# Optimization experiments

Hardware: AMD Instinct MI355X
Metric: run time of the kernel (lower is better)

Reference implementation:

```python
import jax, jax.numpy as jnp
import numpy as np

N_NODES = 10000
N_EDGES = 320000
OBS_DIM = 30
ACT_DIM = 4
HID = 128


def setup_inputs() -> dict:
    key = jax.random.key(0)
    ks = jax.random.split(key, 16)

    def lin(k, fan_in, fan_out):
        s = 1.0 / np.sqrt(fan_in)
        kw, kb = jax.random.split(k)
        w = jax.random.uniform(kw, (fan_in, fan_out), jnp.float32, -s, s)
        b = jax.random.uniform(kb, (fan_out,), jnp.float32, -s, s)
        return w, b

    obs = jax.random.normal(ks[0], (N_NODES, OBS_DIM), jnp.float32)
    action = jax.random.normal(ks[1], (N_NODES, ACT_DIM), jnp.float32)
    edge_index = jax.random.randint(ks[2], (2, N_EDGES), 0, N_NODES, jnp.int64)

    w_g1, b_g1 = lin(ks[3], OBS_DIM + ACT_DIM, HID)
    w_g2, b_g2 = lin(ks[4], HID, HID)
    w_q1a, b_q1a = lin(ks[5], HID, HID)
    w_q1b, b_q1b = lin(ks[6], HID, 1)
    w_q2a, b_q2a = lin(ks[7], HID, HID)
    w_q2b, b_q2b = lin(ks[8], HID, 1)

    return dict(obs=obs, action=action, edge_index=edge_index,
                w_g1=w_g1, b_g1=b_g1, w_g2=w_g2, b_g2=b_g2,
                w_q1a=w_q1a, b_q1a=b_q1a, w_q1b=w_q1b, b_q1b=b_q1b,
                w_q2a=w_q2a, b_q2a=b_q2a, w_q2b=w_q2b, b_q2b=b_q2b)


def gcn_conv(x, w, b, src, dst, deg_inv_sqrt, n):
    xw = x @ w                                      # [N, Fout] small GEMM
    norm = deg_inv_sqrt[src] * deg_inv_sqrt[dst]    # [E'] edge norm
    msg = xw[src] * norm[:, None]                   # gather + scale, [E', Fout]
    out = jax.ops.segment_sum(msg, dst, num_segments=n)  # scatter-add
    return out + b


def reference(obs, action, edge_index,
              w_g1, b_g1, w_g2, b_g2,
              w_q1a, b_q1a, w_q1b, b_q1b,
              w_q2a, b_q2a, w_q2b, b_q2b):
    n = obs.shape[0]
    loops = jnp.arange(n, dtype=edge_index.dtype)
    src = jnp.concatenate([edge_index[0], loops])   # add self-loops
    dst = jnp.concatenate([edge_index[1], loops])

    deg = jnp.zeros((n,), jnp.float32).at[dst].add(1.0)
    deg_inv_sqrt = jnp.where(deg > 0, jax.lax.rsqrt(jnp.maximum(deg, 1.0)), 0.0)

    x = jnp.concatenate([obs, action], axis=1)
    x = jax.nn.relu(gcn_conv(x, w_g1, b_g1, src, dst, deg_inv_sqrt, n))
    x = jax.nn.relu(gcn_conv(x, w_g2, b_g2, src, dst, deg_inv_sqrt, n))

    q1 = jax.nn.relu(x @ w_q1a + b_q1a) @ w_q1b + b_q1b
    q2 = jax.nn.relu(x @ w_q2a + b_q2a) @ w_q2b + b_q2b
    return (q1, q2)
```

## Files before the change

kernel.cpp:

```cpp
#include <hip/hip_runtime.h>

#define N_NODES 10000
#define N_EDGES 320000
#define OBS_DIM 30
#define ACT_DIM 4
#define HID 128
#define ELL_W 96
#define SENT N_NODES


__global__ __launch_bounds__(256) void k_init(int* __restrict__ cnt,
                                              float* __restrict__ xpad,
                                              float* __restrict__ ph1,
                                              const float* __restrict__ obs,
                                              const float* __restrict__ act) {
    int i = blockIdx.x * 256 + threadIdx.x;
    if (i < (N_NODES + 1) * 16) {
        int row = i >> 4, sub = i & 15;
        float4 v = make_float4(0.f, 0.f, 0.f, 0.f);
        if (row < N_NODES) {
            float* vv = &v.x;
#pragma unroll
            for (int k = 0; k < 4; ++k) {
                int c = sub * 4 + k;
                if (c < OBS_DIM) vv[k] = obs[row * OBS_DIM + c];
                else if (c < OBS_DIM + ACT_DIM) vv[k] = act[row * ACT_DIM + (c - OBS_DIM)];
            }
        }
        ((float4*)xpad)[i] = v;
    }
    if (i <= N_NODES) cnt[i] = 0;
    if (i < HID / 4)
        ((float4*)(ph1 + (size_t)SENT * HID))[i] = make_float4(0.f, 0.f, 0.f, 0.f);
}


__global__ __launch_bounds__(256) void k_build(const int4* __restrict__ src4,
                                               const int4* __restrict__ dst4,
                                               int* __restrict__ cnt,
                                               int* __restrict__ col) {
    int i = blockIdx.x * 256 + threadIdx.x;
    if (i < N_EDGES / 4) {
        int4 s = src4[i];
        int4 d = dst4[i];
        int p;
        p = atomicAdd(&cnt[d.x], 1); col[d.x * ELL_W + p] = s.x;
        p = atomicAdd(&cnt[d.y], 1); col[d.y * ELL_W + p] = s.y;
        p = atomicAdd(&cnt[d.z], 1); col[d.z * ELL_W + p] = s.z;
        p = atomicAdd(&cnt[d.w], 1); col[d.w * ELL_W + p] = s.w;
    }
}


__global__ __launch_bounds__(512) void k_l1(const float4* __restrict__ x4,
                                            const int* __restrict__ cnt,
                                            const int* __restrict__ col,
                                            const float* __restrict__ W1,
                                            const float* __restrict__ b1,
                                            float* __restrict__ ph1) {
    __shared__ float w1s[34 * 128];
    __shared__ float zs[8][64];
    int t = threadIdx.x;
    {
        float4* wsp = (float4*)w1s;
        const float4* Wp = (const float4*)W1;
        for (int i = t; i < 1088; i += 512) wsp[i] = Wp[i];
    }
    __syncthreads();
    int wave = t >> 6, lane = t & 63, g = lane >> 4, sub = lane & 15;
    int node = blockIdx.x * 8 + wave;
    int deg = cnt[node];
    float di = rsqrtf((float)(deg + 1));
    const int* cp = col + node * ELL_W;
    float4 a = make_float4(0.f, 0.f, 0.f, 0.f);
    if (g == 0) {
        float4 xv = x4[node * 16 + sub];
        a.x = di * xv.x; a.y = di * xv.y; a.z = di * xv.z; a.w = di * xv.w;
    }
    for (int e = 0; e < deg; e += 8) {
        int s0 = e + g, s1 = e + 4 + g;
        int j0 = (s0 < deg) ? cp[s0] : SENT;
        int j1 = (s1 < deg) ? cp[s1] : SENT;
        float d0 = rsqrtf((float)(cnt[j0] + 1));
        float d1 = rsqrtf((float)(cnt[j1] + 1));
        float4 v0 = x4[j0 * 16 + sub];
        float4 v1 = x4[j1 * 16 + sub];
        a.x += d0 * v0.x + d1 * v1.x;
        a.y += d0 * v0.y + d1 * v1.y;
        a.z += d0 * v0.z + d1 * v1.z;
        a.w += d0 * v0.w + d1 * v1.w;
    }
    a.x += __shfl_xor(a.x, 16); a.x += __shfl_xor(a.x, 32);
    a.y += __shfl_xor(a.y, 16); a.y += __shfl_xor(a.y, 32);
    a.z += __shfl_xor(a.z, 16); a.z += __shfl_xor(a.z, 32);
    a.w += __shfl_xor(a.w, 16); a.w += __shfl_xor(a.w, 32);
    if (g == 0) {
        float4 z;
        z.x = di * a.x; z.y = di * a.y; z.z = di * a.z; z.w = di * a.w;
        *(float4*)&zs[wave][sub * 4] = z;
    }
    float h0 = b1[lane], h64 = b1[lane + 64];
#pragma unroll
    for (int k = 0; k < 34; ++k) {
        float zk = zs[wave][k];
        h0 += zk * w1s[k * 128 + lane];
        h64 += zk * w1s[k * 128 + 64 + lane];
    }
    ph1[node * HID + lane] = di * fmaxf(h0, 0.0f);
    ph1[node * HID + 64 + lane] = di * fmaxf(h64, 0.0f);
}


__global__ __launch_bounds__(256) void k_agg2(const float4* __restrict__ ph14,
                                              const int* __restrict__ cnt,
                                              const int* __restrict__ col,
                                              float4* __restrict__ sbuf) {
    int t = threadIdx.x;
    int wave = t >> 6, lane = t & 63, half = lane >> 5, sub = lane & 31;
    int node = blockIdx.x * 4 + wave;
    int deg = cnt[node];
    const int* cp = col + node * ELL_W;
    float4 a = make_float4(0.f, 0.f, 0.f, 0.f);
    float4 b = make_float4(0.f, 0.f, 0.f, 0.f);
    if (!half) a = ph14[node * 32 + sub];
    for (int e = 0; e < deg; e += 16) {
        int jj[8];
#pragma unroll
        for (int u = 0; u < 8; ++u) {
            int s = e + 2 * u + half;
            jj[u] = (s < deg) ? cp[s] : SENT;
        }
        float4 v0 = ph14[jj[0] * 32 + sub];
        float4 v1 = ph14[jj[1] * 32 + sub];
        float4 v2 = ph14[jj[2] * 32 + sub];
        float4 v3 = ph14[jj[3] * 32 + sub];
        float4 v4 = ph14[jj[4] * 32 + sub];
        float4 v5 = ph14[jj[5] * 32 + sub];
        float4 v6 = ph14[jj[6] * 32 + sub];
        float4 v7 = ph14[jj[7] * 32 + sub];
        a.x += (v0.x + v1.x) + (v2.x + v3.x);
        a.y += (v0.y + v1.y) + (v2.y + v3.y);
        a.z += (v0.z + v1.z) + (v2.z + v3.z);
        a.w += (v0.w + v1.w) + (v2.w + v3.w);
        b.x += (v4.x + v5.x) + (v6.x + v7.x);
        b.y += (v4.y + v5.y) + (v6.y + v7.y);
        b.z += (v4.z + v5.z) + (v6.z + v7.z);
        b.w += (v4.w + v5.w) + (v6.w + v7.w);
    }
    a.x += b.x; a.y += b.y; a.z += b.z; a.w += b.w;
    a.x += __shfl_xor(a.x, 32);
    a.y += __shfl_xor(a.y, 32);
    a.z += __shfl_xor(a.z, 32);
    a.w += __shfl_xor(a.w, 32);
    if (!half) sbuf[node * 32 + sub] = a;
}


__global__ __launch_bounds__(256) void k_h2heads(const float4* __restrict__ sbuf4,
                                                 const int* __restrict__ cnt,
                                                 const float* __restrict__ W2, const float* __restrict__ b2,
                                                 const float* __restrict__ Wq1, const float* __restrict__ Bq1,
                                                 const float* __restrict__ w1b, const float* __restrict__ b1b,
                                                 const float* __restrict__ Wq2, const float* __restrict__ Bq2,
                                                 const float* __restrict__ w2b, const float* __restrict__ b2b,
                                                 float* __restrict__ q1, float* __restrict__ q2) {
    __shared__ float xs[16 * 128];
    __shared__ float hs[16 * 128];
    __shared__ float wbA[32 * 128];
    __shared__ float wbB[32 * 128];
    __shared__ float part1[4][8], part2[4][8];
    int t = threadIdx.x;
    int row0 = blockIdx.x * 16;
    {
        float4* xsp = (float4*)xs;
        for (int i = t; i < 512; i += 256) xsp[i] = sbuf4[row0 * 32 + i];
    }
    int c = t & 127, q = t >> 7;
    float acc[8] = {0, 0, 0, 0, 0, 0, 0, 0};
    for (int ch = 0; ch < 4; ++ch) {
        __syncthreads();
        {
            float4* wp = (float4*)wbA;
            const float4* Wp = (const float4*)(W2 + ch * 4096);
            for (int i = t; i < 1024; i += 256) wp[i] = Wp[i];
        }
        __syncthreads();
        for (int k = 0; k < 32; ++k) {
            float wv = wbA[k * 128 + c];
#pragma unroll
            for (int r = 0; r < 8; ++r)
                acc[r] += xs[(q * 8 + r) * 128 + ch * 32 + k] * wv;
        }
    }
    {
        float bb = b2[c];
#pragma unroll
        for (int r = 0; r < 8; ++r) {
            int row = row0 + q * 8 + r;
            float dr = rsqrtf((float)(cnt[row] + 1));
            hs[(q * 8 + r) * 128 + c] = fmaxf(dr * acc[r] + bb, 0.0f);
        }
    }
    float a1[8] = {0, 0, 0, 0, 0, 0, 0, 0};
    float a2[8] = {0, 0, 0, 0, 0, 0, 0, 0};
    for (int ch = 0; ch < 4; ++ch) {
        __syncthreads();
        {
            float4* w1p = (float4*)wbA;
            float4* w2p = (float4*)wbB;
            const float4* W1p = (const float4*)(Wq1 + ch * 4096);
            const float4* W2p = (const float4*)(Wq2 + ch * 4096);
            for (int i = t; i < 1024; i += 256) {
                w1p[i] = W1p[i];
                w2p[i] = W2p[i];
            }
        }
        __syncthreads();
        for (int k = 0; k < 32; ++k) {
            float wv1 = wbA[k * 128 + c];
            float wv2 = wbB[k * 128 + c];
#pragma unroll
            for (int r = 0; r < 8; ++r) {
                float xv = hs[(q * 8 + r) * 128 + ch * 32 + k];
                a1[r] += xv * wv1;
                a2[r] += xv * wv2;
            }
        }
    }
    float bb1 = Bq1[c], bb2 = Bq2[c];
    float v1 = w1b[c], v2 = w2b[c];
    float s1[8], s2[8];
#pragma unroll
    for (int r = 0; r < 8; ++r) {
        s1[r] = fmaxf(a1[r] + bb1, 0.0f) * v1;
        s2[r] = fmaxf(a2[r] + bb2, 0.0f) * v2;
    }
#pragma unroll
    for (int off = 1; off < 64; off <<= 1) {
#pragma unroll
        for (int r = 0; r < 8; ++r) {
            s1[r] += __shfl_xor(s1[r], off);
            s2[r] += __shfl_xor(s2[r], off);
        }
    }
    int wave = t >> 6, lane = t & 63;
    if (lane == 0) {
#pragma unroll
        for (int r = 0; r < 8; ++r) {
            part1[wave][r] = s1[r];
            part2[wave][r] = s2[r];
        }
    }
    __syncthreads();
    if (t < 16) {
        int hf = t >> 3, r = t & 7;
        int row = row0 + hf * 8 + r;
        q1[row] = part1[hf * 2][r] + part1[hf * 2 + 1][r] + b1b[0];
        q2[row] = part2[hf * 2][r] + part2[hf * 2 + 1][r] + b2b[0];
    }
}

extern "C" void kernel_launch(void* const* d_in, const int* in_sizes, int n_in,
                              void* d_out, int out_size, void* d_ws, size_t ws_size,
                              hipStream_t stream) {
    (void)in_sizes; (void)n_in; (void)out_size; (void)ws_size;
    const float* obs  = (const float*)d_in[0];
    const float* act  = (const float*)d_in[1];
    const int*   ei   = (const int*)d_in[2];
    const int*   src  = ei;
    const int*   dst  = ei + N_EDGES;
    const float* w_g1 = (const float*)d_in[3];
    const float* b_g1 = (const float*)d_in[4];
    const float* w_g2 = (const float*)d_in[5];
    const float* b_g2 = (const float*)d_in[6];
    const float* w_q1a = (const float*)d_in[7];
    const float* b_q1a = (const float*)d_in[8];
    const float* w_q1b = (const float*)d_in[9];
    const float* b_q1b = (const float*)d_in[10];
    const float* w_q2a = (const float*)d_in[11];
    const float* b_q2a = (const float*)d_in[12];
    const float* w_q2b = (const float*)d_in[13];
    const float* b_q2b = (const float*)d_in[14];
    float* out = (float*)d_out;

    char* ws = (char*)d_ws;
    size_t off = 0;
    auto alloc = [&](size_t bytes) {
        void* p = ws + off;
        off = (off + bytes + 255) & ~(size_t)255;
        return p;
    };
    int*   cnt  = (int*)alloc((N_NODES + 1) * 4);
    int*   col  = (int*)alloc((size_t)N_NODES * ELL_W * 4);
    float* xpad = (float*)alloc((size_t)(N_NODES + 1) * 64 * 4);
    float* ph1  = (float*)alloc((size_t)(N_NODES + 1) * HID * 4);
    float* sbuf = (float*)alloc((size_t)N_NODES * HID * 4);

    k_init<<<((N_NODES + 1) * 16 + 255) / 256, 256, 0, stream>>>(cnt, xpad, ph1, obs, act);
    k_build<<<(N_EDGES / 4 + 255) / 256, 256, 0, stream>>>(
        (const int4*)src, (const int4*)dst, cnt, col);
    k_l1<<<1250, 512, 0, stream>>>((const float4*)xpad, cnt, col, w_g1, b_g1, ph1);
    k_agg2<<<2500, 256, 0, stream>>>((const float4*)ph1, cnt, col, (float4*)sbuf);
    k_h2heads<<<625, 256, 0, stream>>>((const float4*)sbuf, cnt,
                                       w_g2, b_g2,
                                       w_q1a, b_q1a, w_q1b, b_q1b,
                                       w_q2a, b_q2a, w_q2b, b_q2b,
                                       out, out + N_NODES);
}
```

Baseline: 104.2 us.

## Retile head MLP kernel to 32 rows per block with 2-column register tiles

After: 95.87 us. 1.09x faster.

```diff
diff --git a/kernel.cpp b/kernel.cpp
--- a/kernel.cpp
+++ b/kernel.cpp
@@ -12,6 +12,7 @@
 __global__ __launch_bounds__(256) void k_init(int* __restrict__ cnt,
                                               float* __restrict__ xpad,
                                               float* __restrict__ ph1,
+                                              float* __restrict__ sbufpad,
                                               const float* __restrict__ obs,
                                               const float* __restrict__ act) {
     int i = blockIdx.x * 256 + threadIdx.x;
@@ -32,6 +33,8 @@
     if (i <= N_NODES) cnt[i] = 0;
     if (i < HID / 4)
         ((float4*)(ph1 + (size_t)SENT * HID))[i] = make_float4(0.f, 0.f, 0.f, 0.f);
+    if (i < 16 * 32)
+        ((float4*)sbufpad)[i] = make_float4(0.f, 0.f, 0.f, 0.f);
 }
 
 
@@ -164,19 +167,21 @@
                                                  const float* __restrict__ Wq2, const float* __restrict__ Bq2,
                                                  const float* __restrict__ w2b, const float* __restrict__ b2b,
                                                  float* __restrict__ q1, float* __restrict__ q2) {
-    __shared__ float xs[16 * 128];
-    __shared__ float hs[16 * 128];
+    __shared__ float xs[32 * 128];
+    __shared__ float hs[32 * 128];
     __shared__ float wbA[32 * 128];
-    __shared__ float wbB[32 * 128];
-    __shared__ float part1[4][8], part2[4][8];
     int t = threadIdx.x;
-    int row0 = blockIdx.x * 16;
+    int row0 = blockIdx.x * 32;
     {
         float4* xsp = (float4*)xs;
-        for (int i = t; i < 512; i += 256) xsp[i] = sbuf4[row0 * 32 + i];
-    }
-    int c = t & 127, q = t >> 7;
-    float acc[8] = {0, 0, 0, 0, 0, 0, 0, 0};
+        for (int i = t; i < 1024; i += 256) xsp[i] = sbuf4[row0 * 32 + i];
+    }
+    int lane = t & 63, wave = t >> 6;
+    int c2 = lane * 2;
+    int r0 = wave * 8;
+    float2 acc[8];
+#pragma unroll
+    for (int r = 0; r < 8; ++r) acc[r] = make_float2(0.f, 0.f);
     for (int ch = 0; ch < 4; ++ch) {
         __syncthreads();
         {
@@ -185,29 +190,45 @@
             for (int i = t; i < 1024; i += 256) wp[i] = Wp[i];
         }
         __syncthreads();
-        for (int k = 0; k < 32; ++k) {
-            float wv = wbA[k * 128 + c];
+        for (int k4 = 0; k4 < 8; ++k4) {
+            float4 xr[8];
 #pragma unroll
             for (int r = 0; r < 8; ++r)
-                acc[r] += xs[(q * 8 + r) * 128 + ch * 32 + k] * wv;
+                xr[r] = *(const float4*)&xs[(r0 + r) * 128 + ch * 32 + k4 * 4];
+#pragma unroll
+            for (int j = 0; j < 4; ++j) {
+                float2 w = *(const float2*)&wbA[(k4 * 4 + j) * 128 + c2];
+#pragma unroll
+                for (int r = 0; r < 8; ++r) {
+                    float xv = (&xr[r].x)[j];
+                    acc[r].x += xv * w.x;
+                    acc[r].y += xv * w.y;
+                }
+            }
         }
     }
     {
-        float bb = b2[c];
+        float bbx = b2[c2], bby = b2[c2 + 1];
 #pragma unroll
         for (int r = 0; r < 8; ++r) {
-            int row = row0 + q * 8 + r;
-            float dr = rsqrtf((float)(cnt[row] + 1));
-            hs[(q * 8 + r) * 128 + c] = fmaxf(dr * acc[r] + bb, 0.0f);
-        }
-    }
-    float a1[8] = {0, 0, 0, 0, 0, 0, 0, 0};
-    float a2[8] = {0, 0, 0, 0, 0, 0, 0, 0};
+            int row = row0 + r0 + r;
+            int rc = (row < N_NODES) ? row : (N_NODES - 1);
+            float dr = rsqrtf((float)(cnt[rc] + 1));
+            hs[(r0 + r) * 128 + c2]     = fmaxf(dr * acc[r].x + bbx, 0.f);
+            hs[(r0 + r) * 128 + c2 + 1] = fmaxf(dr * acc[r].y + bby, 0.f);
+        }
+    }
+    float2 a1[8], a2[8];
+#pragma unroll
+    for (int r = 0; r < 8; ++r) {
+        a1[r] = make_float2(0.f, 0.f);
+        a2[r] = make_float2(0.f, 0.f);
+    }
     for (int ch = 0; ch < 4; ++ch) {
         __syncthreads();
         {
             float4* w1p = (float4*)wbA;
-            float4* w2p = (float4*)wbB;
+            float4* w2p = (float4*)xs;
             const float4* W1p = (const float4*)(Wq1 + ch * 4096);
             const float4* W2p = (const float4*)(Wq2 + ch * 4096);
             for (int i = t; i < 1024; i += 256) {
@@ -216,24 +237,35 @@
             }
         }
         __syncthreads();
-        for (int k = 0; k < 32; ++k) {
-            float wv1 = wbA[k * 128 + c];
-            float wv2 = wbB[k * 128 + c];
-#pragma unroll
-            for (int r = 0; r < 8; ++r) {
-                float xv = hs[(q * 8 + r) * 128 + ch * 32 + k];
-                a1[r] += xv * wv1;
-                a2[r] += xv * wv2;
-            }
-        }
-    }
-    float bb1 = Bq1[c], bb2 = Bq2[c];
-    float v1 = w1b[c], v2 = w2b[c];
+        for (int k4 = 0; k4 < 8; ++k4) {
+            float4 xr[8];
+#pragma unroll
+            for (int r = 0; r < 8; ++r)
+                xr[r] = *(const float4*)&hs[(r0 + r) * 128 + ch * 32 + k4 * 4];
+#pragma unroll
+            for (int j = 0; j < 4; ++j) {
+                float2 wA = *(const float2*)&wbA[(k4 * 4 + j) * 128 + c2];
+                float2 wB = *(const float2*)&xs[(k4 * 4 + j) * 128 + c2];
+#pragma unroll
+                for (int r = 0; r < 8; ++r) {
+                    float xv = (&xr[r].x)[j];
+                    a1[r].x += xv * wA.x;
+                    a1[r].y += xv * wA.y;
+                    a2[r].x += xv * wB.x;
+                    a2[r].y += xv * wB.y;
+                }
+            }
+        }
+    }
+    float B1x = Bq1[c2], B1y = Bq1[c2 + 1];
+    float B2x = Bq2[c2], B2y = Bq2[c2 + 1];
+    float v1x = w1b[c2], v1y = w1b[c2 + 1];
+    float v2x = w2b[c2], v2y = w2b[c2 + 1];
     float s1[8], s2[8];
 #pragma unroll
     for (int r = 0; r < 8; ++r) {
-        s1[r] = fmaxf(a1[r] + bb1, 0.0f) * v1;
-        s2[r] = fmaxf(a2[r] + bb2, 0.0f) * v2;
+        s1[r] = fmaxf(a1[r].x + B1x, 0.f) * v1x + fmaxf(a1[r].y + B1y, 0.f) * v1y;
+        s2[r] = fmaxf(a2[r].x + B2x, 0.f) * v2x + fmaxf(a2[r].y + B2y, 0.f) * v2y;
     }
 #pragma unroll
     for (int off = 1; off < 64; off <<= 1) {
@@ -243,20 +275,16 @@
             s2[r] += __shfl_xor(s2[r], off);
         }
     }
-    int wave = t >> 6, lane = t & 63;
     if (lane == 0) {
+        float bq1 = b1b[0], bq2 = b2b[0];
 #pragma unroll
         for (int r = 0; r < 8; ++r) {
-            part1[wave][r] = s1[r];
-            part2[wave][r] = s2[r];
-        }
-    }
-    __syncthreads();
-    if (t < 16) {
-        int hf = t >> 3, r = t & 7;
-        int row = row0 + hf * 8 + r;
-        q1[row] = part1[hf * 2][r] + part1[hf * 2 + 1][r] + b1b[0];
-        q2[row] = part2[hf * 2][r] + part2[hf * 2 + 1][r] + b2b[0];
+            int row = row0 + r0 + r;
+            if (row < N_NODES) {
+                q1[row] = s1[r] + bq1;
+                q2[row] = s2[r] + bq2;
+            }
+        }
     }
 }
 
@@ -294,14 +322,15 @@
     int*   col  = (int*)alloc((size_t)N_NODES * ELL_W * 4);
     float* xpad = (float*)alloc((size_t)(N_NODES + 1) * 64 * 4);
     float* ph1  = (float*)alloc((size_t)(N_NODES + 1) * HID * 4);
-    float* sbuf = (float*)alloc((size_t)N_NODES * HID * 4);
-
-    k_init<<<((N_NODES + 1) * 16 + 255) / 256, 256, 0, stream>>>(cnt, xpad, ph1, obs, act);
+    float* sbuf = (float*)alloc((size_t)(N_NODES + 16) * HID * 4);
+
+    k_init<<<((N_NODES + 1) * 16 + 255) / 256, 256, 0, stream>>>(
+        cnt, xpad, ph1, sbuf + (size_t)N_NODES * HID, obs, act);
     k_build<<<(N_EDGES / 4 + 255) / 256, 256, 0, stream>>>(
         (const int4*)src, (const int4*)dst, cnt, col);
     k_l1<<<1250, 512, 0, stream>>>((const float4*)xpad, cnt, col, w_g1, b_g1, ph1);
     k_agg2<<<2500, 256, 0, stream>>>((const float4*)ph1, cnt, col, (float4*)sbuf);
-    k_h2heads<<<625, 256, 0, stream>>>((const float4*)sbuf, cnt,
+    k_h2heads<<<313, 256, 0, stream>>>((const float4*)sbuf, cnt,
                                        w_g2, b_g2,
                                        w_q1a, b_q1a, w_q1b, b_q1b,
                                        w_q2a, b_q2a, w_q2b, b_q2b,
```
